# Kernel optimization log

Hardware: AMD Instinct MI355X
Metric: run time of the kernel (lower is better)

Reference implementation:

```python
import jax, jax.numpy as jnp
import numpy as np
from jax.ops import segment_sum, segment_max

N_NODES = 100000
N_EDGES = 1600000


def _glorot(key, shape):
    fan_in, fan_out = shape[0], shape[-1]
    lim = np.sqrt(6.0 / (fan_in + fan_out))
    return jax.random.uniform(key, shape, jnp.float32, -lim, lim)


def setup_inputs() -> dict:
    key = jax.random.key(0)
    ks = jax.random.split(key, 12)
    x = jax.random.normal(ks[0], (N_NODES, 7), jnp.float32)
    edge_index = jax.random.randint(ks[1], (2, N_EDGES), 0, N_NODES, jnp.int64)
    return {
        "x": x,
        "edge_index": edge_index,
        # GCNConv(7, 32)
        "W1": _glorot(ks[2], (7, 32)), "b1": jnp.zeros((32,), jnp.float32),
        # GATConv(32, 64), heads=1
        "W2": _glorot(ks[3], (32, 64)), "a_src2": _glorot(ks[4], (64, 1))[:, 0],
        "a_dst2": _glorot(ks[5], (64, 1))[:, 0], "b2": jnp.zeros((64,), jnp.float32),
        # GCNConv(64, 128)
        "W3": _glorot(ks[6], (64, 128)), "b3": jnp.zeros((128,), jnp.float32),
        # GATConv(128, 2), heads=1
        "W4": _glorot(ks[7], (128, 2)), "a_src4": _glorot(ks[8], (2, 1))[:, 0],
        "a_dst4": _glorot(ks[9], (2, 1))[:, 0], "b4": jnp.zeros((2,), jnp.float32),
    }


def _gcn_conv(x, src, dst, W, b):
    # x' = W x; symmetric normalization with self-loops already in (src, dst)
    h = x @ W
    deg = segment_sum(jnp.ones_like(dst, dtype=h.dtype), dst, num_segments=N_NODES)
    dinv = jnp.where(deg > 0, jax.lax.rsqrt(deg), 0.0)
    norm = dinv[src] * dinv[dst]            # [E]
    msg = norm[:, None] * h[src]            # [E, C]
    return segment_sum(msg, dst, num_segments=N_NODES) + b


def _gat_conv(x, src, dst, W, a_src, a_dst, b, slope=0.2):
    h = x @ W                               # [N, C]
    alpha_src = h @ a_src                   # [N]
    alpha_dst = h @ a_dst                   # [N]
    e = alpha_src[src] + alpha_dst[dst]     # [E]
    e = jnp.where(e > 0, e, slope * e)      # leaky_relu
    # numerically-stable softmax over edges grouped by destination node
    m = segment_max(e, dst, num_segments=N_NODES)
    ex = jnp.exp(e - m[dst])
    denom = segment_sum(ex, dst, num_segments=N_NODES)
    w = ex / (denom[dst] + 1e-16)           # [E]
    out = segment_sum(w[:, None] * h[src], dst, num_segments=N_NODES)
    return out + b


def reference(x, edge_index, W1, b1, W2, a_src2, a_dst2, b2, W3, b3, W4, a_src4, a_dst4, b4):
    # add self-loops once (PyG does it per layer; identical edge set each time)
    loop = jnp.arange(N_NODES, dtype=edge_index.dtype)
    src = jnp.concatenate([edge_index[0], loop])
    dst = jnp.concatenate([edge_index[1], loop])

    h = _gcn_conv(x, src, dst, W1, b1)
    h = jax.nn.relu(h)
    h = _gat_conv(h, src, dst, W2, a_src2, a_dst2, b2)
    h = jax.nn.relu(h)
    h = _gcn_conv(h, src, dst, W3, b3)
    h = jax.nn.relu(h)
    h = _gat_conv(h, src, dst, W4, a_src4, a_dst4, b4)
    return jax.nn.log_softmax(h, axis=1)
```

## Files before the change

### kernel.cpp

```cpp
#include <hip/hip_runtime.h>
#include <hip/hip_bf16.h>

#define NN 100000
#define NE 1600000
#define NT (NN + NE)
#define NBKT 256
#define BSZ 391
#define BCAP 10240

typedef unsigned int u32;
typedef unsigned short u16;

static __device__ __forceinline__ int clampN(int s) {
    return ((unsigned)s < (unsigned)NN) ? s : 0;
}
static __device__ __forceinline__ int ld_src(const int* ei, int is32, int e) {
    return is32 ? ei[e] : ei[2 * e];
}
static __device__ __forceinline__ int ld_dst(const int* ei, int is32, int e) {
    return is32 ? ei[NE + e] : ei[2 * NE + 2 * e];
}
static __device__ __forceinline__ float2 b2x2(u32 u) {
    float2 r;
    r.x = __uint_as_float((u & 0xffffu) << 16);
    r.y = __uint_as_float(u & 0xffff0000u);
    return r;
}
static __device__ __forceinline__ u16 f2bs(float f) {
    union { __hip_bfloat16 b; u16 u; } cv;
    cv.b = __float2bfloat16(f);
    return cv.u;
}
static __device__ __forceinline__ u32 pack2(float x, float y) {
    return ((u32)f2bs(y) << 16) | (u32)f2bs(x);
}
static __device__ __forceinline__ float lrelu_c(float e) {
    e = (e > 0.f) ? e : 0.2f * e;
    return fminf(e, 60.f);
}

#define FMA4(acc, s, v) { acc.x += (s)*(v).x; acc.y += (s)*(v).y; \
                          acc.z += (s)*(v).z; acc.w += (s)*(v).w; }


__global__ void __launch_bounds__(256) k_init(const float* __restrict__ x,
                                              const float* __restrict__ W2,
                                              const float* __restrict__ a2s,
                                              const float* __restrict__ a2d,
                                              const int* __restrict__ ei,
                                              u32* __restrict__ xpb,
                                              float* __restrict__ va2,
                                              float* __restrict__ vd2,
                                              int* __restrict__ flag,
                                              int* __restrict__ gcur) {
    int idx = blockIdx.x * 256 + threadIdx.x;
    if (blockIdx.x == 0) {
        if (threadIdx.x == 0) flag[0] = 0;
        __syncthreads();
        int nz = 0;
        for (int i = threadIdx.x; i < 4096; i += 256) nz |= ei[2 * i + 1];
        if (nz) atomicOr(flag, 1);
        if (threadIdx.x < NBKT) gcur[threadIdx.x] = 0;
    }
    if (blockIdx.x == 1 && threadIdx.x < 64) {
        int t = threadIdx.x;
        if (t < 32) {
            float a = 0.f;
            for (int c = 0; c < 64; c++) a += W2[t * 64 + c] * a2s[c];
            va2[t] = a;
        } else {
            int k = t - 32;
            float a = 0.f;
            for (int c = 0; c < 64; c++) a += W2[k * 64 + c] * a2d[c];
            vd2[k] = a;
        }
    }
    if (idx < NN * 4) {
        int n = idx >> 2, c2 = idx & 3;
        float f0 = x[n * 7 + 2 * c2];
        float f1 = (2 * c2 + 1 < 7) ? x[n * 7 + 2 * c2 + 1] : 0.f;
        xpb[idx] = pack2(f0, f1);
    }
}


__global__ void __launch_bounds__(256) k_binA(const int* __restrict__ ei,
                                              const int* __restrict__ flag,
                                              int* __restrict__ gcur,
                                              u32* __restrict__ staging) {
    __shared__ int hist[NBKT];
    __shared__ int gbase[NBKT];
    __shared__ int cnt2[NBKT];
    int tid = threadIdx.x;
    if (tid < NBKT) hist[tid] = 0;
    __syncthreads();

    int base = blockIdx.x * 4096;
    int is32 = flag[0];
    int d[16], s[16];
    #pragma unroll
    for (int i = 0; i < 16; i++) {
        int e = base + i * 256 + tid;
        d[i] = -1;
        if (e < NE) {
            int dd = ld_dst(ei, is32, e);
            if ((unsigned)dd < (unsigned)NN) { d[i] = dd; s[i] = clampN(ld_src(ei, is32, e)); }
        } else if (e < NT) {
            d[i] = e - NE; s[i] = e - NE;
        }
        if (d[i] >= 0) atomicAdd(&hist[d[i] / BSZ], 1);
    }
    __syncthreads();
    if (tid < NBKT) {
        int c = hist[tid];
        gbase[tid] = c ? atomicAdd(&gcur[tid], c) : 0;
        cnt2[tid] = 0;
    }
    __syncthreads();
    #pragma unroll
    for (int i = 0; i < 16; i++) {
        if (d[i] >= 0) {
            int b = d[i] / BSZ;
            int pos = gbase[b] + atomicAdd(&cnt2[b], 1);
            if (pos < BCAP)
                staging[(size_t)b * BCAP + pos] =
                    ((unsigned)(d[i] - b * BSZ) << 17) | (unsigned)s[i];
        }
    }
}

__global__ void __launch_bounds__(256) k_histscan(const u32* __restrict__ staging,
                                                  const int* __restrict__ gcur,
                                                  int* __restrict__ rowptr,
                                                  int* __restrict__ deg,
                                                  int* __restrict__ part) {
    __shared__ int h[512];
    __shared__ int sm[256];
    int b = blockIdx.x, tid = threadIdx.x;
    h[tid] = 0; h[tid + 256] = 0;
    __syncthreads();
    int cnt = min(gcur[b], BCAP);
    const u32* st = staging + (size_t)b * BCAP;
    for (int i = tid; i < cnt; i += 256)
        atomicAdd(&h[st[i] >> 17], 1);
    __syncthreads();
    int h0 = h[2 * tid], h1 = h[2 * tid + 1];
    int pair = h0 + h1;
    sm[tid] = pair;
    __syncthreads();
    for (int off = 1; off < 256; off <<= 1) {
        int t = (tid >= off) ? sm[tid - off] : 0;
        __syncthreads();
        sm[tid] += t;
        __syncthreads();
    }
    int excl = sm[tid] - pair;
    int g0 = b * BSZ + 2 * tid;
    if (2 * tid < BSZ && g0 < NN) { rowptr[g0] = excl; deg[g0] = h0; }
    int g1 = g0 + 1;
    if (2 * tid + 1 < BSZ && g1 < NN) { rowptr[g1] = excl + h0; deg[g1] = h1; }
    if (tid == 255) part[b] = sm[255];
}

__global__ void k_scan2(int* __restrict__ part, int* __restrict__ rowptr) {
    __shared__ int sm[256];
    int t = threadIdx.x;
    int v = part[t];
    sm[t] = v;
    __syncthreads();
    for (int off = 1; off < 256; off <<= 1) {
        int u = (t >= off) ? sm[t - off] : 0;
        __syncthreads();
        sm[t] += u;
        __syncthreads();
    }
    part[t] = sm[t] - v;
    if (t == 0) rowptr[NN] = NT;
}

__global__ void __launch_bounds__(256) k_scat(const u32* __restrict__ staging,
                                              const int* __restrict__ gcur,
                                              const int* __restrict__ part,
                                              int* __restrict__ rowptr,
                                              const int* __restrict__ deg,
                                              float* __restrict__ dinv,
                                              int* __restrict__ col) {
    __shared__ int cur[BSZ];
    int b = blockIdx.x;
    int pb = part[b];
    for (int l = threadIdx.x; l < BSZ; l += 256) {
        int g = b * BSZ + l;
        if (g < NN) {
            int r = rowptr[g] + pb;
            rowptr[g] = r;
            cur[l] = r;
            int d = deg[g];
            dinv[g] = rsqrtf((float)(d > 0 ? d : 1));
        } else cur[l] = 0;
    }
    __syncthreads();
    int cnt = min(gcur[b], BCAP);
    const u32* st = staging + (size_t)b * BCAP;
    for (int i = threadIdx.x; i < cnt; i += 256) {
        u32 w = st[i];
        int l = w >> 17;
        int s = w & 0x1FFFF;
        int p = atomicAdd(&cur[l], 1);
        if ((unsigned)p < (unsigned)NT) col[p] = s;
    }
}


__global__ void __launch_bounds__(256) k_l1(const u32* __restrict__ xpb,
                                            const int* __restrict__ rowptr,
                                            const int* __restrict__ col,
                                            const float* __restrict__ dinv,
                                            const float* __restrict__ W1,
                                            const float* __restrict__ b1,
                                            const float* __restrict__ va2,
                                            const float* __restrict__ vd2,
                                            u32* __restrict__ O1b,
                                            float* __restrict__ as_,
                                            float* __restrict__ ad_) {
    __shared__ float sW1[7 * 32];
    __shared__ float sb1[32], sva[32], svd[32];
    __shared__ float sT1[64 * 8];
    if (threadIdx.x < 224) sW1[threadIdx.x] = W1[threadIdx.x];
    else {
        int c = threadIdx.x - 224;
        sb1[c] = b1[c]; sva[c] = va2[c]; svd[c] = vd2[c];
    }
    int node_l = threadIdx.x >> 2;
    int lane = threadIdx.x & 3;
    int n = blockIdx.x * 64 + node_l;
    if (n < NN) {
        int beg = rowptr[n], end = rowptr[n + 1];
        float ax = 0.f, ay = 0.f;
        #pragma unroll 4
        for (int e = beg; e < end; e++) {
            int s = clampN(col[e]);
            float w = dinv[s];
            float2 f = b2x2(xpb[(size_t)s * 4 + lane]);
            ax += w * f.x;
            ay += w * f.y;
        }
        float dn = dinv[n];
        sT1[node_l * 8 + lane * 2] = ax * dn;
        sT1[node_l * 8 + lane * 2 + 1] = ay * dn;
    }
    __syncthreads();
    if (n >= NN) return;
    int c8 = lane * 8;
    float4 aA = {0,0,0,0}, aB = {0,0,0,0};
    #pragma unroll
    for (int k = 0; k < 7; k++) {
        float t = sT1[node_l * 8 + k];
        float4 wva = *(const float4*)&sW1[k * 32 + c8];
        float4 wvb = *(const float4*)&sW1[k * 32 + c8 + 4];
        FMA4(aA, t, wva);
        FMA4(aB, t, wvb);
    }
    float o0 = fmaxf(aA.x + sb1[c8], 0.f);
    float o1 = fmaxf(aA.y + sb1[c8 + 1], 0.f);
    float o2 = fmaxf(aA.z + sb1[c8 + 2], 0.f);
    float o3 = fmaxf(aA.w + sb1[c8 + 3], 0.f);
    float o4 = fmaxf(aB.x + sb1[c8 + 4], 0.f);
    float o5 = fmaxf(aB.y + sb1[c8 + 5], 0.f);
    float o6 = fmaxf(aB.z + sb1[c8 + 6], 0.f);
    float o7 = fmaxf(aB.w + sb1[c8 + 7], 0.f);
    uint4 pk = {pack2(o0, o1), pack2(o2, o3), pack2(o4, o5), pack2(o6, o7)};
    *(uint4*)(O1b + (size_t)n * 16 + lane * 4) = pk;
    float vs = o0 * sva[c8] + o1 * sva[c8 + 1] + o2 * sva[c8 + 2] + o3 * sva[c8 + 3]
             + o4 * sva[c8 + 4] + o5 * sva[c8 + 5] + o6 * sva[c8 + 6] + o7 * sva[c8 + 7];
    float vd = o0 * svd[c8] + o1 * svd[c8 + 1] + o2 * svd[c8 + 2] + o3 * svd[c8 + 3]
             + o4 * svd[c8 + 4] + o5 * svd[c8 + 5] + o6 * svd[c8 + 6] + o7 * svd[c8 + 7];
    vs += __shfl_xor(vs, 1, 4); vs += __shfl_xor(vs, 2, 4);
    vd += __shfl_xor(vd, 1, 4); vd += __shfl_xor(vd, 2, 4);
    if (lane == 0) { as_[n] = vs; ad_[n] = vd; }
}


__global__ void __launch_bounds__(256) k_l2(const u32* __restrict__ O1b,
                                            const float* __restrict__ as_,
                                            const float* __restrict__ ad_,
                                            const int* __restrict__ rowptr,
                                            const int* __restrict__ col,
                                            const float* __restrict__ W2,
                                            const float* __restrict__ b2,
                                            const float* __restrict__ dinv,
                                            u32* __restrict__ O2b) {
    __shared__ float sW2[32 * 64];
    __shared__ float sT2[32 * 36];
    __shared__ float sb2[64];
    {
        const float4* g = (const float4*)W2;
        float4* s4 = (float4*)sW2;
        s4[threadIdx.x] = g[threadIdx.x];
        s4[threadIdx.x + 256] = g[threadIdx.x + 256];
    }
    if (threadIdx.x < 64) sb2[threadIdx.x] = b2[threadIdx.x];

    int node_l = threadIdx.x >> 3;
    int lane = threadIdx.x & 7;
    int n = blockIdx.x * 32 + node_l;
    {
        int beg = rowptr[n], end = rowptr[n + 1];
        float adn = ad_[n];
        float den = 0.f;
        float4 acc = {0, 0, 0, 0};
        #pragma unroll 2
        for (int e = beg; e < end; e++) {
            int s = clampN(col[e]);
            float p = __expf(lrelu_c(as_[s] + adn));
            den += p;
            uint2 w = *(const uint2*)(O1b + (size_t)s * 16 + lane * 2);
            float2 f0 = b2x2(w.x), f1 = b2x2(w.y);
            acc.x += p * f0.x; acc.y += p * f0.y; acc.z += p * f1.x; acc.w += p * f1.y;
        }
        float inv = 1.0f / (den + 1e-16f);
        acc.x *= inv; acc.y *= inv; acc.z *= inv; acc.w *= inv;
        *(float4*)&sT2[node_l * 36 + lane * 4] = acc;
    }
    __syncthreads();

    int grp = threadIdx.x >> 4;
    int l = threadIdx.x & 15;
    int c4 = l * 4;
    int lbase = grp * 2;

    float4 acc0 = {0,0,0,0}, acc1 = {0,0,0,0};
    #pragma unroll
    for (int k4 = 0; k4 < 8; k4++) {
        float4 t0 = *(const float4*)&sT2[(lbase + 0) * 36 + 4 * k4];
        float4 t1 = *(const float4*)&sT2[(lbase + 1) * 36 + 4 * k4];
        #pragma unroll
        for (int j = 0; j < 4; j++) {
            float4 wv = *(const float4*)&sW2[(4 * k4 + j) * 64 + c4];
            FMA4(acc0, ((const float*)&t0)[j], wv);
            FMA4(acc1, ((const float*)&t1)[j], wv);
        }
    }
    float4 bb = *(const float4*)&sb2[c4];
    int n0 = blockIdx.x * 32 + lbase;
    float d0 = dinv[n0], d1 = dinv[n0 + 1];
    {
        float o0 = fmaxf(acc0.x + bb.x, 0.f) * d0;
        float o1 = fmaxf(acc0.y + bb.y, 0.f) * d0;
        float o2 = fmaxf(acc0.z + bb.z, 0.f) * d0;
        float o3 = fmaxf(acc0.w + bb.w, 0.f) * d0;
        uint2 pk = {pack2(o0, o1), pack2(o2, o3)};
        *(uint2*)(O2b + (size_t)n0 * 32 + l * 2) = pk;
    }
    {
        float o0 = fmaxf(acc1.x + bb.x, 0.f) * d1;
        float o1 = fmaxf(acc1.y + bb.y, 0.f) * d1;
        float o2 = fmaxf(acc1.z + bb.z, 0.f) * d1;
        float o3 = fmaxf(acc1.w + bb.w, 0.f) * d1;
        uint2 pk = {pack2(o0, o1), pack2(o2, o3)};
        *(uint2*)(O2b + (size_t)(n0 + 1) * 32 + l * 2) = pk;
    }
}


__global__ void __launch_bounds__(256) k_agg3(const u32* __restrict__ O2b,
                                              const int* __restrict__ rowptr,
                                              const int* __restrict__ col,
                                              const float* __restrict__ dinv,
                                              float* __restrict__ T3) {
    int gid = blockIdx.x * 256 + threadIdx.x;
    int n = gid >> 3;
    int lane = gid & 7;
    int beg = rowptr[n], end = rowptr[n + 1];
    float4 accA = {0,0,0,0}, accB = {0,0,0,0};
    #pragma unroll 4
    for (int e = beg; e < end; e++) {
        int s = clampN(col[e]);
        uint4 w = *(const uint4*)(O2b + (size_t)s * 32 + lane * 4);
        float2 f0 = b2x2(w.x), f1 = b2x2(w.y), f2 = b2x2(w.z), f3 = b2x2(w.w);
        accA.x += f0.x; accA.y += f0.y; accA.z += f1.x; accA.w += f1.y;
        accB.x += f2.x; accB.y += f2.y; accB.z += f3.x; accB.w += f3.y;
    }
    float dn = dinv[n];
    accA.x *= dn; accA.y *= dn; accA.z *= dn; accA.w *= dn;
    accB.x *= dn; accB.y *= dn; accB.z *= dn; accB.w *= dn;
    float* dst = T3 + (size_t)n * 64 + lane * 8;
    *(float4*)dst = accA;
    *(float4*)(dst + 4) = accB;
}


__global__ void __launch_bounds__(256) k_mm34(const float* __restrict__ T3,
                                              const float* __restrict__ W3,
                                              const float* __restrict__ b3,
                                              const float* __restrict__ W4,
                                              const float* __restrict__ av4s,
                                              const float* __restrict__ av4d,
                                              float4* __restrict__ h4as,
                                              float* __restrict__ as_,
                                              float* __restrict__ ad_) {
    __shared__ float sW3[64 * 128];
    __shared__ float sT3[32 * 64];
    __shared__ float sW4[128 * 2];
    __shared__ float sb3[128];
    {
        const float4* g = (const float4*)W3;
        float4* s4 = (float4*)sW3;
        #pragma unroll
        for (int i = 0; i < 8; i++) s4[threadIdx.x + 256 * i] = g[threadIdx.x + 256 * i];
    }
    {
        const float4* g = (const float4*)(T3 + (size_t)blockIdx.x * 32 * 64);
        float4* s4 = (float4*)sT3;
        s4[threadIdx.x] = g[threadIdx.x];
        s4[threadIdx.x + 256] = g[threadIdx.x + 256];
    }
    if (threadIdx.x < 128) {
        sb3[threadIdx.x] = b3[threadIdx.x];
        sW4[2 * threadIdx.x] = W4[2 * threadIdx.x];
        sW4[2 * threadIdx.x + 1] = W4[2 * threadIdx.x + 1];
    }
    __syncthreads();

    int w = threadIdx.x >> 6;
    int lane = threadIdx.x & 63;
    int half = lane >> 5;
    int lw = lane & 31;
    int lbase = w * 8 + half * 4;
    int c4 = lw * 4;

    float4 acc0 = {0,0,0,0}, acc1 = {0,0,0,0}, acc2 = {0,0,0,0}, acc3 = {0,0,0,0};
    #pragma unroll 4
    for (int k4 = 0; k4 < 16; k4++) {
        float4 t0 = *(const float4*)&sT3[(lbase + 0) * 64 + 4 * k4];
        float4 t1 = *(const float4*)&sT3[(lbase + 1) * 64 + 4 * k4];
        float4 t2 = *(const float4*)&sT3[(lbase + 2) * 64 + 4 * k4];
        float4 t3 = *(const float4*)&sT3[(lbase + 3) * 64 + 4 * k4];
        #pragma unroll
        for (int j = 0; j < 4; j++) {
            float4 wv = *(const float4*)&sW3[(4 * k4 + j) * 128 + c4];
            FMA4(acc0, ((const float*)&t0)[j], wv);
            FMA4(acc1, ((const float*)&t1)[j], wv);
            FMA4(acc2, ((const float*)&t2)[j], wv);
            FMA4(acc3, ((const float*)&t3)[j], wv);
        }
    }

    float4 bb = *(const float4*)&sb3[c4];
    float w40x = sW4[2 * c4],     w41x = sW4[2 * c4 + 1];
    float w40y = sW4[2 * c4 + 2], w41y = sW4[2 * c4 + 3];
    float w40z = sW4[2 * c4 + 4], w41z = sW4[2 * c4 + 5];
    float w40w = sW4[2 * c4 + 6], w41w = sW4[2 * c4 + 7];
    float av4s0 = av4s[0], av4s1 = av4s[1];
    float av4d0 = av4d[0], av4d1 = av4d[1];

    #pragma unroll
    for (int n = 0; n < 4; n++) {
        float4 a = (n == 0) ? acc0 : (n == 1) ? acc1 : (n == 2) ? acc2 : acc3;
        a.x = fmaxf(a.x + bb.x, 0.f);
        a.y = fmaxf(a.y + bb.y, 0.f);
        a.z = fmaxf(a.z + bb.z, 0.f);
        a.w = fmaxf(a.w + bb.w, 0.f);
        float p0 = a.x * w40x + a.y * w40y + a.z * w40z + a.w * w40w;
        float p1 = a.x * w41x + a.y * w41y + a.z * w41z + a.w * w41w;
        #pragma unroll
        for (int off = 16; off > 0; off >>= 1) {
            p0 += __shfl_down(p0, off, 32);
            p1 += __shfl_down(p1, off, 32);
        }
        if (lw == 0) {
            int gn = blockIdx.x * 32 + lbase + n;
            float asv = p0 * av4s0 + p1 * av4s1;
            float4 pk = {p0, p1, asv, 0.f};
            h4as[gn] = pk;
            as_[gn] = asv;
            ad_[gn] = p0 * av4d0 + p1 * av4d1;
        }
    }
}


__global__ void k_final(const float4* __restrict__ h4as, const float* __restrict__ as_,
                        const float* __restrict__ ad_, const int* __restrict__ rowptr,
                        const int* __restrict__ col, const float* __restrict__ b,
                        float* __restrict__ out) {
    int gid = blockIdx.x * 256 + threadIdx.x;
    int n = gid >> 2;
    if (n >= NN) return;
    int lsub = gid & 3;
    int beg = rowptr[n], end = rowptr[n + 1];
    float adn = ad_[n];
    float den = 0.f, a0 = 0.f, a1 = 0.f;
    for (int e = beg + lsub; e < end; e += 4) {
        int s = clampN(col[e]);
        float4 h = h4as[s];
        float p = __expf(lrelu_c(h.z + adn));
        den += p;
        a0 += p * h.x;
        a1 += p * h.y;
    }
    den += __shfl_xor(den, 1, 4); den += __shfl_xor(den, 2, 4);
    a0  += __shfl_xor(a0, 1, 4);  a0  += __shfl_xor(a0, 2, 4);
    a1  += __shfl_xor(a1, 1, 4);  a1  += __shfl_xor(a1, 2, 4);
    if (lsub == 0) {
        float inv = 1.0f / (den + 1e-16f);
        float v0 = a0 * inv + b[0];
        float v1 = a1 * inv + b[1];
        float mx = fmaxf(v0, v1);
        float lse = mx + logf(__expf(v0 - mx) + __expf(v1 - mx));
        float2 o = {v0 - lse, v1 - lse};
        *(float2*)(out + n * 2) = o;
    }
}

__global__ void k_sentinel(float* __restrict__ out, float v) {
    int i = blockIdx.x * 256 + threadIdx.x;
    if (i < NN * 2) out[i] = v;
}


extern "C" void kernel_launch(void* const* d_in, const int* in_sizes, int n_in,
                              void* d_out, int out_size, void* d_ws, size_t ws_size,
                              hipStream_t stream) {
    const float* x    = (const float*)d_in[0];
    const int* ei     = (const int*)d_in[1];
    const float* W1   = (const float*)d_in[2];
    const float* b1   = (const float*)d_in[3];
    const float* W2   = (const float*)d_in[4];
    const float* a2s  = (const float*)d_in[5];
    const float* a2d  = (const float*)d_in[6];
    const float* b2   = (const float*)d_in[7];
    const float* W3   = (const float*)d_in[8];
    const float* b3   = (const float*)d_in[9];
    const float* W4   = (const float*)d_in[10];
    const float* a4s  = (const float*)d_in[11];
    const float* a4d  = (const float*)d_in[12];
    const float* b4   = (const float*)d_in[13];
    float* out = (float*)d_out;

    char* base = (char*)d_ws;
    size_t off = 0;
    auto alloc = [&](size_t bytes) {
        char* q = base + off;
        off += (bytes + 255) & ~(size_t)255;
        return q;
    };
    float* bufA  = (float*)alloc((size_t)NN * 64 * 4);
    float* bufB  = (float*)alloc((size_t)NN * 64 * 4);
    u32* staging = (u32*)alloc((size_t)NBKT * BCAP * 4);
    int* col     = (int*)alloc((size_t)NT * 4);
    int* rowptr  = (int*)alloc((size_t)(NN + 1) * 4);
    int* deg     = (int*)alloc((size_t)NN * 4);
    float* dinv  = (float*)alloc((size_t)NN * 4);
    float* as_   = (float*)alloc((size_t)NN * 4);
    float* ad_   = (float*)alloc((size_t)NN * 4);
    float4* h4as = (float4*)alloc((size_t)NN * 16);
    int* part    = (int*)alloc(512 * 4);
    int* flag    = (int*)alloc(256);
    int* gcur    = (int*)alloc(NBKT * 4);
    float* va2   = (float*)alloc(32 * 4);
    float* vd2   = (float*)alloc(32 * 4);

    float code = 0.f;
    if (off > ws_size)            code = 1000.f + (float)(ws_size >> 20);
    else if (n_in != 14)          code = 2000.f + 10.f * (float)n_in;
    else if (out_size != NN * 2)  code = 3400.f;
    if (code != 0.f) {
        k_sentinel<<<(NN * 2 + 255) / 256, 256, 0, stream>>>(out, code);
        return;
    }

    const int NTILE = (NT + 4095) / 4096;

    k_init<<<NN * 4 / 256, 256, 0, stream>>>(x, W2, a2s, a2d, ei, (u32*)bufA, va2, vd2,
                                             flag, gcur);
    k_binA<<<NTILE, 256, 0, stream>>>(ei, flag, gcur, staging);
    k_histscan<<<NBKT, 256, 0, stream>>>(staging, gcur, rowptr, deg, part);
    k_scan2<<<1, 256, 0, stream>>>(part, rowptr);
    k_scat<<<NBKT, 256, 0, stream>>>(staging, gcur, part, rowptr, deg, dinv, col);

    k_l1<<<(NN + 63) / 64, 256, 0, stream>>>((const u32*)bufA, rowptr, col, dinv,
                                             W1, b1, va2, vd2, (u32*)bufA, as_, ad_);
    k_l2<<<NN / 32, 256, 0, stream>>>((const u32*)bufA, as_, ad_, rowptr, col,
                                      W2, b2, dinv, (u32*)bufA);
    k_agg3<<<NN * 8 / 256, 256, 0, stream>>>((const u32*)bufA, rowptr, col, dinv, bufB);
    k_mm34<<<NN / 32, 256, 0, stream>>>(bufB, W3, b3, W4, a4s, a4d, h4as, as_, ad_);
    k_final<<<NN * 4 / 256 + 1, 256, 0, stream>>>(h4as, as_, ad_, rowptr, col, b4, out);
}
```

Baseline: 270.4 us.

## Fuse layer-3 aggregation with matmul, fold scan2 into scatter, move x packing

Merges the GCN layer-3 neighbour aggregation into the dense W3/W4 kernel, so the aggregated 64-wide features stay in shared memory rather than making a round trip through global memory. The single-block partition scan kernel is removed and each scatter block recomputes the 256-entry prefix scan itself. The x bf16 packing moves from k_init into k_histscan, which cuts launches, and separate buffers replace the aliased in-place ones. The costs are redundant scan work in every scatter block and a larger 512-thread block with more shared memory in the fused layer-3 kernel, which may lower occupancy.

```diff
diff --git a/kernel.cpp b/kernel.cpp
--- a/kernel.cpp
+++ b/kernel.cpp
@@ -43,17 +43,14 @@
                           acc.z += (s)*(v).z; acc.w += (s)*(v).w; }
 
 
-__global__ void __launch_bounds__(256) k_init(const float* __restrict__ x,
-                                              const float* __restrict__ W2,
+__global__ void __launch_bounds__(256) k_init(const float* __restrict__ W2,
                                               const float* __restrict__ a2s,
                                               const float* __restrict__ a2d,
                                               const int* __restrict__ ei,
-                                              u32* __restrict__ xpb,
                                               float* __restrict__ va2,
                                               float* __restrict__ vd2,
                                               int* __restrict__ flag,
                                               int* __restrict__ gcur) {
-    int idx = blockIdx.x * 256 + threadIdx.x;
     if (blockIdx.x == 0) {
         if (threadIdx.x == 0) flag[0] = 0;
         __syncthreads();
@@ -61,8 +58,7 @@
         for (int i = threadIdx.x; i < 4096; i += 256) nz |= ei[2 * i + 1];
         if (nz) atomicOr(flag, 1);
         if (threadIdx.x < NBKT) gcur[threadIdx.x] = 0;
-    }
-    if (blockIdx.x == 1 && threadIdx.x < 64) {
+    } else if (threadIdx.x < 64) {
         int t = threadIdx.x;
         if (t < 32) {
             float a = 0.f;
@@ -74,12 +70,6 @@
             for (int c = 0; c < 64; c++) a += W2[k * 64 + c] * a2d[c];
             vd2[k] = a;
         }
-    }
-    if (idx < NN * 4) {
-        int n = idx >> 2, c2 = idx & 3;
-        float f0 = x[n * 7 + 2 * c2];
-        float f1 = (2 * c2 + 1 < 7) ? x[n * 7 + 2 * c2 + 1] : 0.f;
-        xpb[idx] = pack2(f0, f1);
     }
 }
 
@@ -131,6 +121,8 @@
 
 __global__ void __launch_bounds__(256) k_histscan(const u32* __restrict__ staging,
                                                   const int* __restrict__ gcur,
+                                                  const float* __restrict__ x,
+                                                  u32* __restrict__ xpb,
                                                   int* __restrict__ rowptr,
                                                   int* __restrict__ deg,
                                                   int* __restrict__ part) {
@@ -160,22 +152,13 @@
     int g1 = g0 + 1;
     if (2 * tid + 1 < BSZ && g1 < NN) { rowptr[g1] = excl + h0; deg[g1] = h1; }
     if (tid == 255) part[b] = sm[255];
-}
-
-__global__ void k_scan2(int* __restrict__ part, int* __restrict__ rowptr) {
-    __shared__ int sm[256];
-    int t = threadIdx.x;
-    int v = part[t];
-    sm[t] = v;
-    __syncthreads();
-    for (int off = 1; off < 256; off <<= 1) {
-        int u = (t >= off) ? sm[t - off] : 0;
-        __syncthreads();
-        sm[t] += u;
-        __syncthreads();
-    }
-    part[t] = sm[t] - v;
-    if (t == 0) rowptr[NN] = NT;
+
+    for (int i = b * 256 + tid; i < NN * 4; i += NBKT * 256) {
+        int n = i >> 2, c2 = i & 3;
+        float f0 = x[n * 7 + 2 * c2];
+        float f1 = (2 * c2 + 1 < 7) ? x[n * 7 + 2 * c2 + 1] : 0.f;
+        xpb[i] = pack2(f0, f1);
+    }
 }
 
 __global__ void __launch_bounds__(256) k_scat(const u32* __restrict__ staging,
@@ -185,10 +168,21 @@
                                               const int* __restrict__ deg,
                                               float* __restrict__ dinv,
                                               int* __restrict__ col) {
+    __shared__ int sm[256];
     __shared__ int cur[BSZ];
-    int b = blockIdx.x;
-    int pb = part[b];
-    for (int l = threadIdx.x; l < BSZ; l += 256) {
+    int b = blockIdx.x, tid = threadIdx.x;
+    int v = part[tid];
+    sm[tid] = v;
+    __syncthreads();
+    for (int off = 1; off < 256; off <<= 1) {
+        int t = (tid >= off) ? sm[tid - off] : 0;
+        __syncthreads();
+        sm[tid] += t;
+        __syncthreads();
+    }
+    int pb = (b > 0) ? sm[b - 1] : 0;
+    if (b == 0 && tid == 0) rowptr[NN] = NT;
+    for (int l = tid; l < BSZ; l += 256) {
         int g = b * BSZ + l;
         if (g < NN) {
             int r = rowptr[g] + pb;
@@ -201,7 +195,7 @@
     __syncthreads();
     int cnt = min(gcur[b], BCAP);
     const u32* st = staging + (size_t)b * BCAP;
-    for (int i = threadIdx.x; i < cnt; i += 256) {
+    for (int i = tid; i < cnt; i += 256) {
         u32 w = st[i];
         int l = w >> 17;
         int s = w & 0x1FFFF;
@@ -362,69 +356,66 @@
 }
 
 
-__global__ void __launch_bounds__(256) k_agg3(const u32* __restrict__ O2b,
-                                              const int* __restrict__ rowptr,
-                                              const int* __restrict__ col,
-                                              const float* __restrict__ dinv,
-                                              float* __restrict__ T3) {
-    int gid = blockIdx.x * 256 + threadIdx.x;
-    int n = gid >> 3;
-    int lane = gid & 7;
-    int beg = rowptr[n], end = rowptr[n + 1];
-    float4 accA = {0,0,0,0}, accB = {0,0,0,0};
-    #pragma unroll 4
-    for (int e = beg; e < end; e++) {
-        int s = clampN(col[e]);
-        uint4 w = *(const uint4*)(O2b + (size_t)s * 32 + lane * 4);
-        float2 f0 = b2x2(w.x), f1 = b2x2(w.y), f2 = b2x2(w.z), f3 = b2x2(w.w);
-        accA.x += f0.x; accA.y += f0.y; accA.z += f1.x; accA.w += f1.y;
-        accB.x += f2.x; accB.y += f2.y; accB.z += f3.x; accB.w += f3.y;
-    }
-    float dn = dinv[n];
-    accA.x *= dn; accA.y *= dn; accA.z *= dn; accA.w *= dn;
-    accB.x *= dn; accB.y *= dn; accB.z *= dn; accB.w *= dn;
-    float* dst = T3 + (size_t)n * 64 + lane * 8;
-    *(float4*)dst = accA;
-    *(float4*)(dst + 4) = accB;
-}
-
-
-__global__ void __launch_bounds__(256) k_mm34(const float* __restrict__ T3,
-                                              const float* __restrict__ W3,
-                                              const float* __restrict__ b3,
-                                              const float* __restrict__ W4,
-                                              const float* __restrict__ av4s,
-                                              const float* __restrict__ av4d,
-                                              float4* __restrict__ h4as,
-                                              float* __restrict__ as_,
-                                              float* __restrict__ ad_) {
+__global__ void __launch_bounds__(512) k_l3(const u32* __restrict__ O2b,
+                                            const int* __restrict__ rowptr,
+                                            const int* __restrict__ col,
+                                            const float* __restrict__ dinv,
+                                            const float* __restrict__ W3,
+                                            const float* __restrict__ b3,
+                                            const float* __restrict__ W4,
+                                            const float* __restrict__ av4s,
+                                            const float* __restrict__ av4d,
+                                            float4* __restrict__ h4as,
+                                            float* __restrict__ ad_) {
     __shared__ float sW3[64 * 128];
-    __shared__ float sT3[32 * 64];
+    __shared__ float sT3[64 * 64];
     __shared__ float sW4[128 * 2];
     __shared__ float sb3[128];
+
+    float4 wreg[4];
     {
         const float4* g = (const float4*)W3;
-        float4* s4 = (float4*)sW3;
         #pragma unroll
-        for (int i = 0; i < 8; i++) s4[threadIdx.x + 256 * i] = g[threadIdx.x + 256 * i];
-    }
-    {
-        const float4* g = (const float4*)(T3 + (size_t)blockIdx.x * 32 * 64);
-        float4* s4 = (float4*)sT3;
-        s4[threadIdx.x] = g[threadIdx.x];
-        s4[threadIdx.x + 256] = g[threadIdx.x + 256];
+        for (int i = 0; i < 4; i++) wreg[i] = g[threadIdx.x + 512 * i];
     }
     if (threadIdx.x < 128) {
         sb3[threadIdx.x] = b3[threadIdx.x];
         sW4[2 * threadIdx.x] = W4[2 * threadIdx.x];
         sW4[2 * threadIdx.x + 1] = W4[2 * threadIdx.x + 1];
     }
+
+    int node_l = threadIdx.x >> 3;
+    int lane = threadIdx.x & 7;
+    int n = blockIdx.x * 64 + node_l;
+    if (n < NN) {
+        int beg = rowptr[n], end = rowptr[n + 1];
+        float4 accA = {0,0,0,0}, accB = {0,0,0,0};
+        #pragma unroll 4
+        for (int e = beg; e < end; e++) {
+            int s = clampN(col[e]);
+            uint4 w = *(const uint4*)(O2b + (size_t)s * 32 + lane * 4);
+            float2 f0 = b2x2(w.x), f1 = b2x2(w.y), f2 = b2x2(w.z), f3 = b2x2(w.w);
+            accA.x += f0.x; accA.y += f0.y; accA.z += f1.x; accA.w += f1.y;
+            accB.x += f2.x; accB.y += f2.y; accB.z += f3.x; accB.w += f3.y;
+        }
+        float dn = dinv[n];
+        accA.x *= dn; accA.y *= dn; accA.z *= dn; accA.w *= dn;
+        accB.x *= dn; accB.y *= dn; accB.z *= dn; accB.w *= dn;
+        float* dst = &sT3[node_l * 64 + lane * 8];
+        *(float4*)dst = accA;
+        *(float4*)(dst + 4) = accB;
+    }
+    {
+        float4* s4 = (float4*)sW3;
+        #pragma unroll
+        for (int i = 0; i < 4; i++) s4[threadIdx.x + 512 * i] = wreg[i];
+    }
     __syncthreads();
 
     int w = threadIdx.x >> 6;
-    int lane = threadIdx.x & 63;
-    int half = lane >> 5;
-    int lw = lane & 31;
+    int lane64 = threadIdx.x & 63;
+    int half = lane64 >> 5;
+    int lw = lane64 & 31;
     int lbase = w * 8 + half * 4;
     int c4 = lw * 4;
 
@@ -454,8 +445,8 @@
     float av4d0 = av4d[0], av4d1 = av4d[1];
 
     #pragma unroll
-    for (int n = 0; n < 4; n++) {
-        float4 a = (n == 0) ? acc0 : (n == 1) ? acc1 : (n == 2) ? acc2 : acc3;
+    for (int ni = 0; ni < 4; ni++) {
+        float4 a = (ni == 0) ? acc0 : (ni == 1) ? acc1 : (ni == 2) ? acc2 : acc3;
         a.x = fmaxf(a.x + bb.x, 0.f);
         a.y = fmaxf(a.y + bb.y, 0.f);
         a.z = fmaxf(a.z + bb.z, 0.f);
@@ -468,18 +459,19 @@
             p1 += __shfl_down(p1, off, 32);
         }
         if (lw == 0) {
-            int gn = blockIdx.x * 32 + lbase + n;
-            float asv = p0 * av4s0 + p1 * av4s1;
-            float4 pk = {p0, p1, asv, 0.f};
-            h4as[gn] = pk;
-            as_[gn] = asv;
-            ad_[gn] = p0 * av4d0 + p1 * av4d1;
-        }
-    }
-}
-
-
-__global__ void k_final(const float4* __restrict__ h4as, const float* __restrict__ as_,
+            int gn = blockIdx.x * 64 + lbase + ni;
+            if (gn < NN) {
+                float asv = p0 * av4s0 + p1 * av4s1;
+                float4 pk = {p0, p1, asv, 0.f};
+                h4as[gn] = pk;
+                ad_[gn] = p0 * av4d0 + p1 * av4d1;
+            }
+        }
+    }
+}
+
+
+__global__ void k_final(const float4* __restrict__ h4as,
                         const float* __restrict__ ad_, const int* __restrict__ rowptr,
                         const int* __restrict__ col, const float* __restrict__ b,
                         float* __restrict__ out) {
@@ -544,8 +536,9 @@
         off += (bytes + 255) & ~(size_t)255;
         return q;
     };
-    float* bufA  = (float*)alloc((size_t)NN * 64 * 4);
-    float* bufB  = (float*)alloc((size_t)NN * 64 * 4);
+    u32* xpb     = (u32*)alloc((size_t)NN * 4 * 4);
+    u32* O1b     = (u32*)alloc((size_t)NN * 16 * 4);
+    u32* O2b     = (u32*)alloc((size_t)NN * 32 * 4);
     u32* staging = (u32*)alloc((size_t)NBKT * BCAP * 4);
     int* col     = (int*)alloc((size_t)NT * 4);
     int* rowptr  = (int*)alloc((size_t)(NN + 1) * 4);
@@ -571,18 +564,16 @@
 
     const int NTILE = (NT + 4095) / 4096;
 
-    k_init<<<NN * 4 / 256, 256, 0, stream>>>(x, W2, a2s, a2d, ei, (u32*)bufA, va2, vd2,
-                                             flag, gcur);
+    k_init<<<2, 256, 0, stream>>>(W2, a2s, a2d, ei, va2, vd2, flag, gcur);
     k_binA<<<NTILE, 256, 0, stream>>>(ei, flag, gcur, staging);
-    k_histscan<<<NBKT, 256, 0, stream>>>(staging, gcur, rowptr, deg, part);
-    k_scan2<<<1, 256, 0, stream>>>(part, rowptr);
+    k_histscan<<<NBKT, 256, 0, stream>>>(staging, gcur, x, xpb, rowptr, deg, part);
     k_scat<<<NBKT, 256, 0, stream>>>(staging, gcur, part, rowptr, deg, dinv, col);
 
-    k_l1<<<(NN + 63) / 64, 256, 0, stream>>>((const u32*)bufA, rowptr, col, dinv,
-                                             W1, b1, va2, vd2, (u32*)bufA, as_, ad_);
-    k_l2<<<NN / 32, 256, 0, stream>>>((const u32*)bufA, as_, ad_, rowptr, col,
-                                      W2, b2, dinv, (u32*)bufA);
-    k_agg3<<<NN * 8 / 256, 256, 0, stream>>>((const u32*)bufA, rowptr, col, dinv, bufB);
-    k_mm34<<<NN / 32, 256, 0, stream>>>(bufB, W3, b3, W4, a4s, a4d, h4as, as_, ad_);
-    k_final<<<NN * 4 / 256 + 1, 256, 0, stream>>>(h4as, as_, ad_, rowptr, col, b4, out);
-}
+    k_l1<<<(NN + 63) / 64, 256, 0, stream>>>(xpb, rowptr, col, dinv,
+                                             W1, b1, va2, vd2, O1b, as_, ad_);
+    k_l2<<<NN / 32, 256, 0, stream>>>(O1b, as_, ad_, rowptr, col,
+                                      W2, b2, dinv, O2b);
+    k_l3<<<(NN + 63) / 64, 512, 0, stream>>>(O2b, rowptr, col, dinv,
+                                             W3, b3, W4, a4s, a4d, h4as, ad_);
+    k_final<<<NN * 4 / 256 + 1, 256, 0, stream>>>(h4as, ad_, rowptr, col, b4, out);
+}
```

New measurement: 258.0 us. 4.6% less time.
